# Kernel optimization log

Hardware: AMD Instinct MI355X
Metric: run time of the kernel (lower is better)

Reference implementation:

```python
import jax, jax.numpy as jnp
import numpy as np

N = 20000       # nodes
E = 100000      # edges
STEPS = 4
ND = 128        # node feature dim
ED = 128        # edge feature dim
NIN = 128       # node input dim
EIN = 291       # edge input dim (2 + 17*17)
H = 64          # mpn edge-mlp hidden


def _lin(x, w, b):
    return x @ w + b


def setup_inputs():
    key = jax.random.key(0)
    ks = jax.random.split(key, 16)

    def w(k, i, o):
        return (jax.random.normal(k, (i, o), jnp.float32) / np.float32(np.sqrt(i)))

    d = {}
    d["x"] = jax.random.normal(ks[0], (N, NIN), jnp.float32)
    d["edge_attr"] = jax.random.normal(ks[1], (E, EIN), jnp.float32)
    d["edge_index"] = jax.random.randint(ks[2], (2, E), 0, N, jnp.int32)
    # node embedding MLP: NIN -> 128 -> ND (ReLU between, none after last)
    d["new0"] = w(ks[3], NIN, 128); d["neb0"] = jnp.zeros(128, jnp.float32)
    d["new1"] = w(ks[4], 128, ND); d["neb1"] = jnp.zeros(ND, jnp.float32)
    # edge embedding MLP: EIN -> 64 -> ED
    d["eew0"] = w(ks[5], EIN, 64); d["eeb0"] = jnp.zeros(64, jnp.float32)
    d["eew1"] = w(ks[6], 64, ED); d["eeb1"] = jnp.zeros(ED, jnp.float32)
    # MPN edge MLP (skip=True): 2*(2*ND) + 2*ED = 768 -> 64 -> ED, ReLU after each
    d["mew0"] = w(ks[7], 4 * ND + 2 * ED, H); d["meb0"] = jnp.zeros(H, jnp.float32)
    d["mew1"] = w(ks[8], H, ED); d["meb1"] = jnp.zeros(ED, jnp.float32)
    # MPN node MLP: 2*ND + ED = 384 -> ND, ReLU
    d["mnw0"] = w(ks[9], 2 * ND + ED, ND); d["mnb0"] = jnp.zeros(ND, jnp.float32)
    # classification MLP: ED -> 64 -> 32 -> 1
    d["cw0"] = w(ks[10], ED, 64); d["cb0"] = jnp.zeros(64, jnp.float32)
    d["cw1"] = w(ks[11], 64, 32); d["cb1"] = jnp.zeros(32, jnp.float32)
    d["cw2"] = w(ks[12], 32, 1); d["cb2"] = jnp.zeros(1, jnp.float32)
    return d


def reference(x, edge_attr, edge_index,
              new0, neb0, new1, neb1,
              eew0, eeb0, eew1, eeb1,
              mew0, meb0, mew1, meb1,
              mnw0, mnb0,
              cw0, cb0, cw1, cb1, cw2, cb2):
    relu = jax.nn.relu
    j, i = edge_index[0], edge_index[1]  # j: source, i: target

    nf = _lin(relu(_lin(x, new0, neb0)), new1, neb1)          # [N, ND]
    ef = _lin(relu(_lin(edge_attr, eew0, eeb0)), eew1, eeb1)  # [E, ED]
    nf0, ef0 = nf, ef

    for _ in range(STEPS):
        # skip connections: concat initial features
        nfc = jnp.concatenate([nf0, nf], axis=1)  # [N, 2*ND]
        efc = jnp.concatenate([ef0, ef], axis=1)  # [E, 2*ED]
        x_i = nfc[i]  # [E, 2*ND] target
        x_j = nfc[j]  # [E, 2*ND] source
        # edge update MLP (ReLU after both layers)
        h = relu(_lin(jnp.concatenate([x_i, x_j, efc], axis=1), mew0, meb0))
        ef = relu(_lin(h, mew1, meb1))  # [E, ED]
        # message: mlp_node([x_i, edge_attr_new]) aggregated at target i
        msg = relu(_lin(jnp.concatenate([x_i, ef], axis=1), mnw0, mnb0))  # [E, ND]
        nf = jax.ops.segment_sum(msg, i, num_segments=N)  # [N, ND]

    out = relu(_lin(ef, cw0, cb0))
    out = relu(_lin(out, cw1, cb1))
    out = _lin(out, cw2, cb2)  # [E, 1]
    return out
```

## Files before the change

kernel.cpp:

```cpp
#include <hip/hip_runtime.h>
#include <hip/hip_bf16.h>

#define ND 128
#define ED 128
#define NIN 128
#define EIN 291
#define KPAD 320
#define HH 64
#define TM 32
#define TS 64
#define GSE 768
#define MAXGE 3

typedef __attribute__((ext_vector_type(8))) short short8;
typedef __attribute__((ext_vector_type(4))) float float4_;

__device__ __forceinline__ unsigned short f2bf(float f)
{
    union { float f; unsigned u; } v; v.f = f;
    unsigned u = v.u;
    unsigned r = (u + 0x7FFFu + ((u >> 16) & 1u)) >> 16;
    return (unsigned short)r;
}
__device__ __forceinline__ float bf2f(unsigned short s)
{
    union { unsigned u; float f; } v; v.u = ((unsigned)s) << 16;
    return v.f;
}

template<int T, int KC, int K>
__device__ __forceinline__ void stage_frags(const unsigned short* __restrict__ src,
                                            unsigned short* __restrict__ wreg,
                                            int t, int k0)
{
    constexpr int TOT = T * KC * 64;
#pragma unroll
    for (int it = 0; it < TOT / 256; it++) {
        int idx = it * 256 + t;
        int f = idx >> 6, l = idx & 63;
        int col = (f / KC) * 16 + (l & 15);
        int k = (f % KC) * 32 + ((l >> 4) * 8);
        *(short8*)&wreg[idx * 8] = *(const short8*)&src[(size_t)col * K + k0 + k];
    }
}
#define FRAG(wreg, f, lane) (*(const short8*)&(wreg)[(((f) << 6) + (lane)) * 8])

__global__ __launch_bounds__(256) void zero_k(float* __restrict__ p, int n4)
{
    int idx = blockIdx.x * 256 + threadIdx.x;
    if (idx < n4) ((float4*)p)[idx] = make_float4(0.f, 0.f, 0.f, 0.f);
}

__global__ __launch_bounds__(256) void hist_k(const int* __restrict__ tgti,
                                              int* __restrict__ deg, int E)
{
    int e = blockIdx.x * 256 + threadIdx.x;
    if (e < E) atomicAdd(&deg[tgti[e]], 1);
}

__global__ __launch_bounds__(256) void scan_k(const int* __restrict__ deg,
                                              int* __restrict__ row_ptr,
                                              int* __restrict__ cursor, int N, int E)
{
    __shared__ int part[256];
    const int t = threadIdx.x;
    const int chunk = (N + 255) / 256;
    const int base = t * chunk;
    int s = 0;
    for (int k = 0; k < chunk; k++) { int idx = base + k; if (idx < N) s += deg[idx]; }
    part[t] = s;
    __syncthreads();
    for (int off = 1; off < 256; off <<= 1) {
        int v = (t >= off) ? part[t - off] : 0;
        __syncthreads();
        part[t] += v;
        __syncthreads();
    }
    int run = (t == 0) ? 0 : part[t - 1];
    for (int k = 0; k < chunk; k++) {
        int idx = base + k;
        if (idx < N) { row_ptr[idx] = run; cursor[idx] = run; run += deg[idx]; }
    }
    if (t == 255) row_ptr[N] = E;
}

__global__ __launch_bounds__(256) void scatter_k(const int* __restrict__ tgti,
                                                 int* __restrict__ cursor,
                                                 int* __restrict__ csr_eid, int E)
{
    int e = blockIdx.x * 256 + threadIdx.x;
    if (e < E) {
        int p = atomicAdd(&cursor[tgti[e]], 1);
        csr_eid[p] = e;
    }
}

__global__ __launch_bounds__(256) void permidx_k(const int* __restrict__ csr_eid,
                                                 const int* __restrict__ srcj,
                                                 const int* __restrict__ tgti,
                                                 int* __restrict__ srcp,
                                                 int* __restrict__ tgtp, int E)
{
    int p = blockIdx.x * 256 + threadIdx.x;
    if (p < E) {
        int e = csr_eid[p];
        srcp[p] = srcj[e];
        tgtp[p] = tgti[e];
    }
}

__global__ __launch_bounds__(256) void fixup_k(const int* __restrict__ row_ptr,
                                               float* __restrict__ nfx,
                                               unsigned short* __restrict__ nf_out, int N)
{
    int n = blockIdx.x * 2 + (threadIdx.x >> 7);
    int c = threadIdx.x & 127;
    if (n >= N) return;
    int beg = row_ptr[n], end = row_ptr[n + 1];
    if (beg == end) { nf_out[(size_t)n * ND + c] = 0; return; }
    if ((beg >> 5) != ((end - 1) >> 5)) {
        size_t idx = (size_t)n * ND + c;
        nf_out[idx] = f2bf(nfx[idx]);
        nfx[idx] = 0.f;
    }
}

__global__ __launch_bounds__(256) void wprep_k(
    const float* __restrict__ mew0, const float* __restrict__ mew1, const float* __restrict__ mnw0,
    const float* __restrict__ eew0, const float* __restrict__ eew1, const float* __restrict__ cw0,
    const float* __restrict__ new0, const float* __restrict__ new1,
    unsigned short* __restrict__ w0T, unsigned short* __restrict__ w1T,
    unsigned short* __restrict__ wmT, unsigned short* __restrict__ w0eT,
    unsigned short* __restrict__ w1eT, unsigned short* __restrict__ cw0T,
    unsigned short* __restrict__ w0nT, unsigned short* __restrict__ w1nT)
{
    int idx = blockIdx.x * 256 + threadIdx.x;
    if (idx < 49152) {
        int c = idx / 768, k = idx % 768;
        w0T[idx] = f2bf(mew0[k * 64 + c]);
    } else if (idx < 57344) {
        int j = idx - 49152; int c = j / 64, k = j % 64;
        w1T[j] = f2bf(mew1[k * 128 + c]);
    } else if (idx < 106496) {
        int j = idx - 57344; int c = j / 384, k = j % 384;
        wmT[j] = f2bf(mnw0[k * 128 + c]);
    } else if (idx < 126976) {
        int j = idx - 106496; int c = j / KPAD, k = j % KPAD;
        w0eT[j] = (k < EIN) ? f2bf(eew0[k * 64 + c]) : (unsigned short)0;
    } else if (idx < 135168) {
        int j = idx - 126976; int c = j / 64, k = j % 64;
        w1eT[j] = f2bf(eew1[k * 128 + c]);
    } else if (idx < 143360) {
        int j = idx - 135168; int c = j / 128, k = j % 128;
        cw0T[j] = f2bf(cw0[k * 64 + c]);
    } else if (idx < 159744) {
        int j = idx - 143360; int c = j / 128, k = j % 128;
        w0nT[j] = f2bf(new0[k * 128 + c]);
    } else if (idx < 176128) {
        int j = idx - 159744; int c = j / 128, k = j % 128;
        w1nT[j] = f2bf(new1[k * 128 + c]);
    }
}

__global__ __launch_bounds__(256) void node_embed_k(
    const float* __restrict__ x,
    const unsigned short* __restrict__ w0nT, const float* __restrict__ b0,
    const unsigned short* __restrict__ w1nT, const float* __restrict__ b1,
    unsigned short* __restrict__ nf0_bf, unsigned short* __restrict__ nf_bf, int N)
{
    const int t = threadIdx.x;
    const int n0 = blockIdx.x * TM;
    __shared__ unsigned short wreg[8192];
    __shared__ unsigned short xin[TM][130];
    __shared__ unsigned short h_bf[TM][130];

#pragma unroll
    for (int it = 0; it < 4; it++) {
        int idx = it * 256 + t;
        int r = idx >> 5, c4 = idx & 31;
        int node = n0 + r; if (node >= N) node = N - 1;
        float4 v = *(const float4*)(x + (size_t)node * NIN + c4 * 4);
        unsigned lo = (unsigned)f2bf(v.x) | ((unsigned)f2bf(v.y) << 16);
        unsigned hi = (unsigned)f2bf(v.z) | ((unsigned)f2bf(v.w) << 16);
        *(uint2*)&xin[r][c4 * 4] = make_uint2(lo, hi);
    }

    const int w = t >> 6, lane = t & 63, quad = lane >> 4, n16 = lane & 15;
    const int m = w & 1, nh = w >> 1;

    float4_ acc[4];
#pragma unroll
    for (int q = 0; q < 4; q++) acc[q] = (float4_){0.f, 0.f, 0.f, 0.f};
#pragma unroll
    for (int hf = 0; hf < 2; hf++) {
        stage_frags<8, 2, 128>(w0nT, wreg, t, hf * 64);
        __syncthreads();
#pragma unroll
        for (int kc = 0; kc < 2; kc++) {
            short8 a = *(const short8*)&xin[m * 16 + n16][hf * 64 + kc * 32 + quad * 8];
#pragma unroll
            for (int tt = 0; tt < 4; tt++) {
                short8 b = FRAG(wreg, (nh * 4 + tt) * 2 + kc, lane);
                acc[tt] = __builtin_amdgcn_mfma_f32_16x16x32_bf16(a, b, acc[tt], 0, 0, 0);
            }
        }
        __syncthreads();
    }
#pragma unroll
    for (int tt = 0; tt < 4; tt++) {
        int c = nh * 64 + tt * 16 + n16;
        float bias = b0[c];
#pragma unroll
        for (int r4 = 0; r4 < 4; r4++)
            h_bf[m * 16 + quad * 4 + r4][c] = f2bf(fmaxf(acc[tt][r4] + bias, 0.f));
    }
    __syncthreads();

    float4_ acc2[4];
#pragma unroll
    for (int q = 0; q < 4; q++) acc2[q] = (float4_){0.f, 0.f, 0.f, 0.f};
#pragma unroll
    for (int hf = 0; hf < 2; hf++) {
        stage_frags<8, 2, 128>(w1nT, wreg, t, hf * 64);
        __syncthreads();
#pragma unroll
        for (int kc = 0; kc < 2; kc++) {
            short8 a = *(const short8*)&h_bf[m * 16 + n16][hf * 64 + kc * 32 + quad * 8];
#pragma unroll
            for (int tt = 0; tt < 4; tt++) {
                short8 b = FRAG(wreg, (nh * 4 + tt) * 2 + kc, lane);
                acc2[tt] = __builtin_amdgcn_mfma_f32_16x16x32_bf16(a, b, acc2[tt], 0, 0, 0);
            }
        }
        __syncthreads();
    }
#pragma unroll
    for (int tt = 0; tt < 4; tt++) {
        int c = nh * 64 + tt * 16 + n16;
        float bias = b1[c];
#pragma unroll
        for (int r4 = 0; r4 < 4; r4++) {
            int row = m * 16 + quad * 4 + r4;
            int node = n0 + row;
            if (node < N) {
                unsigned short v = f2bf(acc2[tt][r4] + bias);
                nf0_bf[(size_t)node * ND + c] = v;
                nf_bf[(size_t)node * ND + c] = v;
            }
        }
    }
}

__global__ __launch_bounds__(256, 3) void edge_embed_k(
    const float* __restrict__ ea, const int* __restrict__ csr_eid,
    const unsigned short* __restrict__ w0eT, const float* __restrict__ b0,
    const unsigned short* __restrict__ w1eT, const float* __restrict__ b1,
    unsigned short* __restrict__ ef0_bf, unsigned short* __restrict__ ef_bf,
    int E, int ntiles)
{
    const int t = threadIdx.x;
    __shared__ unsigned short w0reg[10240];
    __shared__ unsigned short w1reg[8192];
    __shared__ unsigned short hsl[4][16 * 66];

    const int w = t >> 6, lane = t & 63, quad = lane >> 4, n16 = lane & 15;

    stage_frags<8, 2, 64>(w1eT, w1reg, t, 0);

    int ng = 0;
    int tile[MAXGE];
#pragma unroll
    for (int g = 0; g < MAXGE; g++) {
        int tl = blockIdx.x + g * GSE;
        if (tl < ntiles) { tile[g] = tl; ng = g + 1; }
        else tile[g] = 0;
    }

    float4_ accL[MAXGE][4];
#pragma unroll
    for (int g = 0; g < MAXGE; g++)
#pragma unroll
        for (int q = 0; q < 4; q++) accL[g][q] = (float4_){0.f, 0.f, 0.f, 0.f};

#pragma unroll
    for (int hf = 0; hf < 2; hf++) {
        __syncthreads();
        stage_frags<4, 5, KPAD>(w0eT, w0reg, t, hf * 160);
        __syncthreads();
#pragma unroll
        for (int g = 0; g < MAXGE; g++) {
            if (g < ng) {
                int p = tile[g] * 64 + w * 16 + n16; if (p >= E) p = E - 1;
                const float* src = ea + (size_t)csr_eid[p] * EIN;
#pragma unroll
                for (int kc = 0; kc < 5; kc++) {
                    int k = hf * 160 + kc * 32 + quad * 8;
                    union { short8 s; uint4 u; } av;
                    if (k + 8 <= EIN) {
                        float4 v0 = *(const float4*)(src + k);
                        float4 v1 = *(const float4*)(src + k + 4);
                        av.u.x = (unsigned)f2bf(v0.x) | ((unsigned)f2bf(v0.y) << 16);
                        av.u.y = (unsigned)f2bf(v0.z) | ((unsigned)f2bf(v0.w) << 16);
                        av.u.z = (unsigned)f2bf(v1.x) | ((unsigned)f2bf(v1.y) << 16);
                        av.u.w = (unsigned)f2bf(v1.z) | ((unsigned)f2bf(v1.w) << 16);
                    } else {
                        unsigned short vv[8];
#pragma unroll
                        for (int j = 0; j < 8; j++)
                            vv[j] = (k + j < EIN) ? f2bf(src[k + j]) : (unsigned short)0;
                        av.u.x = (unsigned)vv[0] | ((unsigned)vv[1] << 16);
                        av.u.y = (unsigned)vv[2] | ((unsigned)vv[3] << 16);
                        av.u.z = (unsigned)vv[4] | ((unsigned)vv[5] << 16);
                        av.u.w = (unsigned)vv[6] | ((unsigned)vv[7] << 16);
                    }
#pragma unroll
                    for (int tt = 0; tt < 4; tt++) {
                        short8 b = FRAG(w0reg, tt * 5 + kc, lane);
                        accL[g][tt] = __builtin_amdgcn_mfma_f32_16x16x32_bf16(av.s, b, accL[g][tt], 0, 0, 0);
                    }
                }
            }
        }
    }

#pragma unroll
    for (int g = 0; g < MAXGE; g++) {
        if (g < ng) {
#pragma unroll
            for (int tt = 0; tt < 4; tt++) {
                int c = tt * 16 + n16;
                float bias = b0[c];
#pragma unroll
                for (int r4 = 0; r4 < 4; r4++)
                    hsl[w][(quad * 4 + r4) * 66 + c] = f2bf(fmaxf(accL[g][tt][r4] + bias, 0.f));
            }
            float4_ acc2[8];
#pragma unroll
            for (int q = 0; q < 8; q++) acc2[q] = (float4_){0.f, 0.f, 0.f, 0.f};
#pragma unroll
            for (int kc = 0; kc < 2; kc++) {
                short8 a2 = *(const short8*)&hsl[w][n16 * 66 + kc * 32 + quad * 8];
#pragma unroll
                for (int tt = 0; tt < 8; tt++)
                    acc2[tt] = __builtin_amdgcn_mfma_f32_16x16x32_bf16(
                        a2, FRAG(w1reg, tt * 2 + kc, lane), acc2[tt], 0, 0, 0);
            }
#pragma unroll
            for (int tt = 0; tt < 8; tt++) {
                int c = tt * 16 + n16;
                float bias = b1[c];
#pragma unroll
                for (int r4 = 0; r4 < 4; r4++) {
                    int p = tile[g] * 64 + w * 16 + quad * 4 + r4;
                    if (p < E) {
                        unsigned short v = f2bf(acc2[tt][r4] + bias);
                        ef0_bf[(size_t)p * ED + c] = v;
                        ef_bf[(size_t)p * ED + c] = v;
                    }
                }
            }
        }
    }
}

__global__ __launch_bounds__(256, 4) void edge_step_k(
    const int* __restrict__ srcp, const int* __restrict__ tgtp,
    const unsigned short* __restrict__ nf0_bf, const unsigned short* __restrict__ nf_in,
    const unsigned short* __restrict__ ef0_bf, unsigned short* __restrict__ ef_bf,
    unsigned short* __restrict__ nf_out, float* __restrict__ nfx,
    const unsigned short* __restrict__ w0T, const float* __restrict__ meb0,
    const unsigned short* __restrict__ w1T, const float* __restrict__ meb1,
    const unsigned short* __restrict__ wmT, const float* __restrict__ mnb0,
    int E, int wmsg)
{
    const int t = threadIdx.x;
    const int e0 = blockIdx.x * TS;
    __shared__ unsigned short wreg[8192];
    __shared__ unsigned short hef[4][2080];

    const int w = t >> 6, lane = t & 63, quad = lane >> 4, n16 = lane & 15;
    int ec = e0 + w * 16 + n16; if (ec >= E) ec = E - 1;
    const int ti = tgtp[ec], sj = srcp[ec];

    const unsigned short* pA[6] = {
        nf0_bf + (size_t)ti * ND + quad * 8,
        nf_in  + (size_t)ti * ND + quad * 8,
        nf0_bf + (size_t)sj * ND + quad * 8,
        nf_in  + (size_t)sj * ND + quad * 8,
        ef0_bf + (size_t)ec * ED + quad * 8,
        ef_bf  + (size_t)ec * ED + quad * 8 };

    float4_ accL[4];
#pragma unroll
    for (int q = 0; q < 4; q++) accL[q] = (float4_){0.f, 0.f, 0.f, 0.f};
#pragma unroll
    for (int hf = 0; hf < 6; hf++) {
        short8 a4[4];
#pragma unroll
        for (int q2 = 0; q2 < 4; q2++)
            a4[q2] = *(const short8*)(pA[hf] + q2 * 32);
        stage_frags<4, 4, 768>(w0T, wreg, t, hf * 128);
        __syncthreads();
#pragma unroll
        for (int kc = 0; kc < 4; kc++) {
#pragma unroll
            for (int tt = 0; tt < 4; tt++) {
                short8 b = FRAG(wreg, tt * 4 + kc, lane);
                accL[tt] = __builtin_amdgcn_mfma_f32_16x16x32_bf16(a4[kc], b, accL[tt], 0, 0, 0);
            }
        }
        __syncthreads();
    }

#pragma unroll
    for (int tt = 0; tt < 4; tt++) {
        int c = tt * 16 + n16;
        float bias = meb0[c];
#pragma unroll
        for (int r4 = 0; r4 < 4; r4++)
            hef[w][(quad * 4 + r4) * 66 + c] = f2bf(fmaxf(accL[tt][r4] + bias, 0.f));
    }

    stage_frags<8, 2, 64>(w1T, wreg, t, 0);
    __syncthreads();
    {
        float4_ acc[8];
#pragma unroll
        for (int q = 0; q < 8; q++) acc[q] = (float4_){0.f, 0.f, 0.f, 0.f};
#pragma unroll
        for (int kc = 0; kc < 2; kc++) {
            short8 a = *(const short8*)&hef[w][n16 * 66 + kc * 32 + quad * 8];
#pragma unroll
            for (int tt = 0; tt < 8; tt++) {
                short8 b = FRAG(wreg, tt * 2 + kc, lane);
                acc[tt] = __builtin_amdgcn_mfma_f32_16x16x32_bf16(a, b, acc[tt], 0, 0, 0);
            }
        }
#pragma unroll
        for (int tt = 0; tt < 8; tt++) {
            int c = tt * 16 + n16;
            float bias = meb1[c];
#pragma unroll
            for (int r4 = 0; r4 < 4; r4++) {
                int row = quad * 4 + r4;
                unsigned short v = f2bf(fmaxf(acc[tt][r4] + bias, 0.f));
                hef[w][row * 130 + c] = v;
                int e = e0 + w * 16 + row;
                if (e < E) ef_bf[(size_t)e * ED + c] = v;
            }
        }
    }
    __syncthreads();

    if (wmsg) {
        float4_ accM[8];
#pragma unroll
        for (int q = 0; q < 8; q++) accM[q] = (float4_){0.f, 0.f, 0.f, 0.f};
#pragma unroll
        for (int j = 0; j < 6; j++) {
            short8 a2[2];
#pragma unroll
            for (int kc = 0; kc < 2; kc++) {
                int kk = j * 2 + kc;
                if (kk < 8) a2[kc] = *(const short8*)(pA[kk >> 2] + (kk & 3) * 32);
                else        a2[kc] = *(const short8*)&hef[w][n16 * 130 + (kk - 8) * 32 + quad * 8];
            }
            stage_frags<8, 2, 384>(wmT, wreg, t, j * 64);
            __syncthreads();
#pragma unroll
            for (int kc = 0; kc < 2; kc++) {
#pragma unroll
                for (int tt = 0; tt < 8; tt++) {
                    short8 b = FRAG(wreg, tt * 2 + kc, lane);
                    accM[tt] = __builtin_amdgcn_mfma_f32_16x16x32_bf16(a2[kc], b, accM[tt], 0, 0, 0);
                }
            }
            __syncthreads();
        }

#pragma unroll
        for (int tt = 0; tt < 8; tt++) {
            int c = tt * 16 + n16;
            float bias = mnb0[c];
#pragma unroll
            for (int r4 = 0; r4 < 4; r4++) {
                int row = w * 16 + quad * 4 + r4;
                wreg[row * 128 + c] = f2bf(fmaxf(accM[tt][r4] + bias, 0.f));
            }
        }
        int* tg = (int*)&hef[0][0];
        if (t < 66) {
            int p = e0 - 1 + t;
            tg[t] = (p >= 0 && p < E) ? tgtp[p] : -1;
        }
        __syncthreads();
        {
            int c = t & 127, half = t >> 7;
            int r0 = half * 32;
            float acc = 0.f;
            int rs = 0;
            for (int r = 0; r < 32; r++) {
                int p = e0 + r0 + r;
                if (p >= E) break;
                int n = tg[r0 + r + 1];
                acc += bf2f(wreg[(r0 + r) * 128 + c]);
                bool end_here = (tg[r0 + r + 2] != n);
                if (end_here) {
                    bool beg_in = (rs > 0) || (tg[r0] != n);
                    if (beg_in) nf_out[(size_t)n * ND + c] = f2bf(acc);
                    else        atomicAdd(&nfx[(size_t)n * ND + c], acc);
                    acc = 0.f; rs = r + 1;
                } else if (r == 31) {
                    atomicAdd(&nfx[(size_t)n * ND + c], acc);
                }
            }
        }
    }
}

__global__ __launch_bounds__(256) void classify_k(
    const unsigned short* __restrict__ ef_bf, const int* __restrict__ csr_eid,
    const unsigned short* __restrict__ cw0T, const float* __restrict__ cb0,
    const float* __restrict__ cw1, const float* __restrict__ cb1,
    const float* __restrict__ cw2, const float* __restrict__ cb2,
    float* __restrict__ out, int E)
{
    const int t = threadIdx.x;
    const int e0 = blockIdx.x * TM;
    __shared__ unsigned short h0_bf[TM][66];
    __shared__ float h1[TM][33];

    const int w = t >> 6, lane = t & 63, quad = lane >> 4, n16 = lane & 15;
    const int m = w & 1;
    const int erow = m * 16 + n16;
    int ec = e0 + erow; if (ec >= E) ec = E - 1;
    const unsigned short* pa = ef_bf + (size_t)ec * ED + quad * 8;

    {
        const int cb = (w >> 1) * 32;
        float4_ acc0 = {0.f, 0.f, 0.f, 0.f}, acc1 = acc0;
        const unsigned short* b0p = cw0T + (size_t)(cb + n16) * 128 + quad * 8;
        const unsigned short* b1p = b0p + (size_t)16 * 128;
#pragma unroll
        for (int kc = 0; kc < 4; kc++) {
            short8 a  = *(const short8*)(pa + kc * 32);
            short8 bb0 = *(const short8*)(b0p + kc * 32);
            short8 bb1 = *(const short8*)(b1p + kc * 32);
            acc0 = __builtin_amdgcn_mfma_f32_16x16x32_bf16(a, bb0, acc0, 0, 0, 0);
            acc1 = __builtin_amdgcn_mfma_f32_16x16x32_bf16(a, bb1, acc1, 0, 0, 0);
        }
#pragma unroll
        for (int t2 = 0; t2 < 2; t2++) {
            int c = cb + t2 * 16 + n16;
            float bias = cb0[c];
            float4_ ac = t2 ? acc1 : acc0;
#pragma unroll
            for (int r4 = 0; r4 < 4; r4++)
                h0_bf[m * 16 + quad * 4 + r4][c] = f2bf(fmaxf(ac[r4] + bias, 0.f));
        }
    }
    __syncthreads();

    {
        int c = t & 31;
        int rbase = (t >> 5) * 4;
#pragma unroll
        for (int q = 0; q < 4; q++) {
            int r = rbase + q;
            float acc = cb1[c];
#pragma unroll 8
            for (int k = 0; k < 64; k++) acc += bf2f(h0_bf[r][k]) * cw1[k * 32 + c];
            h1[r][c] = fmaxf(acc, 0.f);
        }
    }
    __syncthreads();

    if (t < TM) {
        int p = e0 + t;
        if (p < E) {
            float a = cb2[0];
#pragma unroll
            for (int k = 0; k < 32; k++) a += h1[t][k] * cw2[k];
            out[csr_eid[p]] = a;
        }
    }
}

extern "C" void kernel_launch(void* const* d_in, const int* in_sizes, int n_in,
                              void* d_out, int out_size, void* d_ws, size_t ws_size,
                              hipStream_t stream)
{
    const float* x    = (const float*)d_in[0];
    const float* ea   = (const float*)d_in[1];
    const int*   eidx = (const int*)d_in[2];
    const float* new0 = (const float*)d_in[3];  const float* neb0 = (const float*)d_in[4];
    const float* new1 = (const float*)d_in[5];  const float* neb1 = (const float*)d_in[6];
    const float* eew0 = (const float*)d_in[7];  const float* eeb0 = (const float*)d_in[8];
    const float* eew1 = (const float*)d_in[9];  const float* eeb1 = (const float*)d_in[10];
    const float* mew0 = (const float*)d_in[11]; const float* meb0 = (const float*)d_in[12];
    const float* mew1 = (const float*)d_in[13]; const float* meb1 = (const float*)d_in[14];
    const float* mnw0 = (const float*)d_in[15]; const float* mnb0 = (const float*)d_in[16];
    const float* cw0  = (const float*)d_in[17]; const float* cb0  = (const float*)d_in[18];
    const float* cw1  = (const float*)d_in[19]; const float* cb1  = (const float*)d_in[20];
    const float* cw2  = (const float*)d_in[21]; const float* cb2  = (const float*)d_in[22];

    const int N = in_sizes[0] / NIN;
    const int E = in_sizes[2] / 2;
    const int* srcj = eidx;
    const int* tgti = eidx + E;

    char* wsb = (char*)d_ws;
    unsigned short* nf0_bf = (unsigned short*)wsb;
    unsigned short* nfA    = nf0_bf + (size_t)N * ND;
    unsigned short* ef0_bf = nfA + (size_t)N * ND;
    unsigned short* ef_bf  = ef0_bf + (size_t)E * ED;
    unsigned short* slot   = ef_bf + (size_t)E * ED;
    unsigned short* nfB    = slot;
    float*          nfx    = (float*)(slot + (size_t)N * ND);
    unsigned short* w0T  = slot + (size_t)E * ND;
    unsigned short* w1T  = w0T + 49152;
    unsigned short* wmT  = w1T + 8192;
    unsigned short* w0eT = wmT + 49152;
    unsigned short* w1eT = w0eT + 64 * KPAD;
    unsigned short* cw0T = w1eT + 8192;
    unsigned short* w0nT = cw0T + 8192;
    unsigned short* w1nT = w0nT + 16384;
    int* deg     = (int*)(w1nT + 16384);
    int* cursor  = deg + N;
    int* row_ptr = cursor + N;
    int* csr_eid = row_ptr + (N + 4);
    int* srcp    = csr_eid + E;
    int* tgtp    = srcp + E;

    const int eblocks32 = (E + TM - 1) / TM;
    const int nblocks32 = (N + TM - 1) / TM;
    const int ntiles64 = (E + 63) / 64;

    wprep_k<<<(176128 + 255) / 256, 256, 0, stream>>>(mew0, mew1, mnw0, eew0, eew1, cw0,
                                                      new0, new1,
                                                      w0T, w1T, wmT, w0eT, w1eT, cw0T,
                                                      w0nT, w1nT);

    zero_k<<<((2 * N) / 4 + 255) / 256, 256, 0, stream>>>((float*)deg, (2 * N) / 4);
    hist_k<<<(E + 255) / 256, 256, 0, stream>>>(tgti, deg, E);
    scan_k<<<1, 256, 0, stream>>>(deg, row_ptr, cursor, N, E);
    scatter_k<<<(E + 255) / 256, 256, 0, stream>>>(tgti, cursor, csr_eid, E);
    permidx_k<<<(E + 255) / 256, 256, 0, stream>>>(csr_eid, srcj, tgti, srcp, tgtp, E);

    zero_k<<<((N * ND) / 4 + 255) / 256, 256, 0, stream>>>(nfx, (N * ND) / 4);

    node_embed_k<<<nblocks32, 256, 0, stream>>>(x, w0nT, neb0, w1nT, neb1,
                                                nf0_bf, nfA, N);
    edge_embed_k<<<GSE, 256, 0, stream>>>(ea, csr_eid, w0eT, eeb0, w1eT, eeb1,
                                          ef0_bf, ef_bf, E, ntiles64);

    unsigned short* nfR = nfA;
    unsigned short* nfW = nfB;
    for (int s = 0; s < 4; s++) {
        edge_step_k<<<ntiles64, 256, 0, stream>>>(srcp, tgtp, nf0_bf, nfR,
                                                  ef0_bf, ef_bf, nfW, nfx,
                                                  w0T, meb0, w1T, meb1, wmT, mnb0,
                                                  E, (s < 3) ? 1 : 0);
        if (s < 3) {
            fixup_k<<<(N + 1) / 2, 256, 0, stream>>>(row_ptr, nfx, nfW, N);
            unsigned short* tmp = nfR; nfR = nfW; nfW = tmp;
        }
    }

    classify_k<<<eblocks32, 256, 0, stream>>>(ef_bf, csr_eid, cw0T, cb0, cw1, cb1, cw2, cb2,
                                              (float*)d_out, E);
}
```

Before: 664.0 us.

## Merge node and edge embedding kernels and fold setup launches together

Several launches are combined. The deg zeroing moves into the weight-prep kernel, the permuted-index writes move into the scatter kernel, and node and edge embedding become one kernel that picks its branch by block index and shares one shared-memory buffer. The goal is to cut launch count and gaps between kernels, and to let the small node-embedding work run beside the edge embedding. One catch is that the fused embed kernel carries the edge path's launch bound of 3 and its larger shared-memory footprint, which may lower occupancy for the node blocks.

```diff
diff --git a/kernel.cpp b/kernel.cpp
--- a/kernel.cpp
+++ b/kernel.cpp
@@ -84,28 +84,20 @@
     if (t == 255) row_ptr[N] = E;
 }
 
-__global__ __launch_bounds__(256) void scatter_k(const int* __restrict__ tgti,
+__global__ __launch_bounds__(256) void scatter_k(const int* __restrict__ srcj,
+                                                 const int* __restrict__ tgti,
                                                  int* __restrict__ cursor,
-                                                 int* __restrict__ csr_eid, int E)
+                                                 int* __restrict__ csr_eid,
+                                                 int* __restrict__ srcp,
+                                                 int* __restrict__ tgtp, int E)
 {
     int e = blockIdx.x * 256 + threadIdx.x;
     if (e < E) {
-        int p = atomicAdd(&cursor[tgti[e]], 1);
+        int tg = tgti[e];
+        int p = atomicAdd(&cursor[tg], 1);
         csr_eid[p] = e;
-    }
-}
-
-__global__ __launch_bounds__(256) void permidx_k(const int* __restrict__ csr_eid,
-                                                 const int* __restrict__ srcj,
-                                                 const int* __restrict__ tgti,
-                                                 int* __restrict__ srcp,
-                                                 int* __restrict__ tgtp, int E)
-{
-    int p = blockIdx.x * 256 + threadIdx.x;
-    if (p < E) {
-        int e = csr_eid[p];
         srcp[p] = srcj[e];
-        tgtp[p] = tgti[e];
+        tgtp[p] = tg;
     }
 }
 
@@ -132,7 +124,8 @@
     unsigned short* __restrict__ w0T, unsigned short* __restrict__ w1T,
     unsigned short* __restrict__ wmT, unsigned short* __restrict__ w0eT,
     unsigned short* __restrict__ w1eT, unsigned short* __restrict__ cw0T,
-    unsigned short* __restrict__ w0nT, unsigned short* __restrict__ w1nT)
+    unsigned short* __restrict__ w0nT, unsigned short* __restrict__ w1nT,
+    int* __restrict__ deg, int N)
 {
     int idx = blockIdx.x * 256 + threadIdx.x;
     if (idx < 49152) {
@@ -159,204 +152,204 @@
     } else if (idx < 176128) {
         int j = idx - 159744; int c = j / 128, k = j % 128;
         w1nT[j] = f2bf(new1[k * 128 + c]);
-    }
-}
-
-__global__ __launch_bounds__(256) void node_embed_k(
+    } else if (idx < 176128 + N) {
+        deg[idx - 176128] = 0;
+    }
+}
+
+__global__ __launch_bounds__(256, 3) void embed_k(
+    const float* __restrict__ ea, const int* __restrict__ csr_eid,
+    const unsigned short* __restrict__ w0eT, const float* __restrict__ eb0,
+    const unsigned short* __restrict__ w1eT, const float* __restrict__ eb1,
+    unsigned short* __restrict__ ef0_bf, unsigned short* __restrict__ ef_bf,
+    int E, int ntiles,
     const float* __restrict__ x,
-    const unsigned short* __restrict__ w0nT, const float* __restrict__ b0,
-    const unsigned short* __restrict__ w1nT, const float* __restrict__ b1,
+    const unsigned short* __restrict__ w0nT, const float* __restrict__ nb0,
+    const unsigned short* __restrict__ w1nT, const float* __restrict__ nb1,
     unsigned short* __restrict__ nf0_bf, unsigned short* __restrict__ nf_bf, int N)
 {
+    __shared__ unsigned short smem[22656];
     const int t = threadIdx.x;
-    const int n0 = blockIdx.x * TM;
-    __shared__ unsigned short wreg[8192];
-    __shared__ unsigned short xin[TM][130];
-    __shared__ unsigned short h_bf[TM][130];
-
-#pragma unroll
-    for (int it = 0; it < 4; it++) {
-        int idx = it * 256 + t;
-        int r = idx >> 5, c4 = idx & 31;
-        int node = n0 + r; if (node >= N) node = N - 1;
-        float4 v = *(const float4*)(x + (size_t)node * NIN + c4 * 4);
-        unsigned lo = (unsigned)f2bf(v.x) | ((unsigned)f2bf(v.y) << 16);
-        unsigned hi = (unsigned)f2bf(v.z) | ((unsigned)f2bf(v.w) << 16);
-        *(uint2*)&xin[r][c4 * 4] = make_uint2(lo, hi);
-    }
-
     const int w = t >> 6, lane = t & 63, quad = lane >> 4, n16 = lane & 15;
-    const int m = w & 1, nh = w >> 1;
-
-    float4_ acc[4];
-#pragma unroll
-    for (int q = 0; q < 4; q++) acc[q] = (float4_){0.f, 0.f, 0.f, 0.f};
-#pragma unroll
-    for (int hf = 0; hf < 2; hf++) {
-        stage_frags<8, 2, 128>(w0nT, wreg, t, hf * 64);
-        __syncthreads();
-#pragma unroll
-        for (int kc = 0; kc < 2; kc++) {
-            short8 a = *(const short8*)&xin[m * 16 + n16][hf * 64 + kc * 32 + quad * 8];
-#pragma unroll
-            for (int tt = 0; tt < 4; tt++) {
-                short8 b = FRAG(wreg, (nh * 4 + tt) * 2 + kc, lane);
-                acc[tt] = __builtin_amdgcn_mfma_f32_16x16x32_bf16(a, b, acc[tt], 0, 0, 0);
-            }
-        }
-        __syncthreads();
-    }
-#pragma unroll
-    for (int tt = 0; tt < 4; tt++) {
-        int c = nh * 64 + tt * 16 + n16;
-        float bias = b0[c];
-#pragma unroll
-        for (int r4 = 0; r4 < 4; r4++)
-            h_bf[m * 16 + quad * 4 + r4][c] = f2bf(fmaxf(acc[tt][r4] + bias, 0.f));
-    }
-    __syncthreads();
-
-    float4_ acc2[4];
-#pragma unroll
-    for (int q = 0; q < 4; q++) acc2[q] = (float4_){0.f, 0.f, 0.f, 0.f};
-#pragma unroll
-    for (int hf = 0; hf < 2; hf++) {
-        stage_frags<8, 2, 128>(w1nT, wreg, t, hf * 64);
-        __syncthreads();
-#pragma unroll
-        for (int kc = 0; kc < 2; kc++) {
-            short8 a = *(const short8*)&h_bf[m * 16 + n16][hf * 64 + kc * 32 + quad * 8];
-#pragma unroll
-            for (int tt = 0; tt < 4; tt++) {
-                short8 b = FRAG(wreg, (nh * 4 + tt) * 2 + kc, lane);
-                acc2[tt] = __builtin_amdgcn_mfma_f32_16x16x32_bf16(a, b, acc2[tt], 0, 0, 0);
-            }
-        }
-        __syncthreads();
-    }
-#pragma unroll
-    for (int tt = 0; tt < 4; tt++) {
-        int c = nh * 64 + tt * 16 + n16;
-        float bias = b1[c];
-#pragma unroll
-        for (int r4 = 0; r4 < 4; r4++) {
-            int row = m * 16 + quad * 4 + r4;
-            int node = n0 + row;
-            if (node < N) {
-                unsigned short v = f2bf(acc2[tt][r4] + bias);
-                nf0_bf[(size_t)node * ND + c] = v;
-                nf_bf[(size_t)node * ND + c] = v;
-            }
-        }
-    }
-}
-
-__global__ __launch_bounds__(256, 3) void edge_embed_k(
-    const float* __restrict__ ea, const int* __restrict__ csr_eid,
-    const unsigned short* __restrict__ w0eT, const float* __restrict__ b0,
-    const unsigned short* __restrict__ w1eT, const float* __restrict__ b1,
-    unsigned short* __restrict__ ef0_bf, unsigned short* __restrict__ ef_bf,
-    int E, int ntiles)
-{
-    const int t = threadIdx.x;
-    __shared__ unsigned short w0reg[10240];
-    __shared__ unsigned short w1reg[8192];
-    __shared__ unsigned short hsl[4][16 * 66];
-
-    const int w = t >> 6, lane = t & 63, quad = lane >> 4, n16 = lane & 15;
-
-    stage_frags<8, 2, 64>(w1eT, w1reg, t, 0);
-
-    int ng = 0;
-    int tile[MAXGE];
-#pragma unroll
-    for (int g = 0; g < MAXGE; g++) {
-        int tl = blockIdx.x + g * GSE;
-        if (tl < ntiles) { tile[g] = tl; ng = g + 1; }
-        else tile[g] = 0;
-    }
-
-    float4_ accL[MAXGE][4];
-#pragma unroll
-    for (int g = 0; g < MAXGE; g++)
-#pragma unroll
-        for (int q = 0; q < 4; q++) accL[g][q] = (float4_){0.f, 0.f, 0.f, 0.f};
-
-#pragma unroll
-    for (int hf = 0; hf < 2; hf++) {
-        __syncthreads();
-        stage_frags<4, 5, KPAD>(w0eT, w0reg, t, hf * 160);
-        __syncthreads();
+
+    if (blockIdx.x < GSE) {
+        unsigned short* w0reg = smem;
+        unsigned short* w1reg = smem + 10240;
+        unsigned short* hsl   = smem + 18432;
+
+        stage_frags<8, 2, 64>(w1eT, w1reg, t, 0);
+
+        int ng = 0;
+        int tile[MAXGE];
+#pragma unroll
+        for (int g = 0; g < MAXGE; g++) {
+            int tl = blockIdx.x + g * GSE;
+            if (tl < ntiles) { tile[g] = tl; ng = g + 1; }
+            else tile[g] = 0;
+        }
+
+        float4_ accL[MAXGE][4];
+#pragma unroll
+        for (int g = 0; g < MAXGE; g++)
+#pragma unroll
+            for (int q = 0; q < 4; q++) accL[g][q] = (float4_){0.f, 0.f, 0.f, 0.f};
+
+#pragma unroll
+        for (int hf = 0; hf < 2; hf++) {
+            __syncthreads();
+            stage_frags<4, 5, KPAD>(w0eT, w0reg, t, hf * 160);
+            __syncthreads();
+#pragma unroll
+            for (int g = 0; g < MAXGE; g++) {
+                if (g < ng) {
+                    int p = tile[g] * 64 + w * 16 + n16; if (p >= E) p = E - 1;
+                    const float* src = ea + (size_t)csr_eid[p] * EIN;
+#pragma unroll
+                    for (int kc = 0; kc < 5; kc++) {
+                        int k = hf * 160 + kc * 32 + quad * 8;
+                        union { short8 s; uint4 u; } av;
+                        if (k + 8 <= EIN) {
+                            float4 v0 = *(const float4*)(src + k);
+                            float4 v1 = *(const float4*)(src + k + 4);
+                            av.u.x = (unsigned)f2bf(v0.x) | ((unsigned)f2bf(v0.y) << 16);
+                            av.u.y = (unsigned)f2bf(v0.z) | ((unsigned)f2bf(v0.w) << 16);
+                            av.u.z = (unsigned)f2bf(v1.x) | ((unsigned)f2bf(v1.y) << 16);
+                            av.u.w = (unsigned)f2bf(v1.z) | ((unsigned)f2bf(v1.w) << 16);
+                        } else {
+                            unsigned short vv[8];
+#pragma unroll
+                            for (int j = 0; j < 8; j++)
+                                vv[j] = (k + j < EIN) ? f2bf(src[k + j]) : (unsigned short)0;
+                            av.u.x = (unsigned)vv[0] | ((unsigned)vv[1] << 16);
+                            av.u.y = (unsigned)vv[2] | ((unsigned)vv[3] << 16);
+                            av.u.z = (unsigned)vv[4] | ((unsigned)vv[5] << 16);
+                            av.u.w = (unsigned)vv[6] | ((unsigned)vv[7] << 16);
+                        }
+#pragma unroll
+                        for (int tt = 0; tt < 4; tt++) {
+                            short8 b = FRAG(w0reg, tt * 5 + kc, lane);
+                            accL[g][tt] = __builtin_amdgcn_mfma_f32_16x16x32_bf16(av.s, b, accL[g][tt], 0, 0, 0);
+                        }
+                    }
+                }
+            }
+        }
+
 #pragma unroll
         for (int g = 0; g < MAXGE; g++) {
             if (g < ng) {
-                int p = tile[g] * 64 + w * 16 + n16; if (p >= E) p = E - 1;
-                const float* src = ea + (size_t)csr_eid[p] * EIN;
-#pragma unroll
-                for (int kc = 0; kc < 5; kc++) {
-                    int k = hf * 160 + kc * 32 + quad * 8;
-                    union { short8 s; uint4 u; } av;
-                    if (k + 8 <= EIN) {
-                        float4 v0 = *(const float4*)(src + k);
-                        float4 v1 = *(const float4*)(src + k + 4);
-                        av.u.x = (unsigned)f2bf(v0.x) | ((unsigned)f2bf(v0.y) << 16);
-                        av.u.y = (unsigned)f2bf(v0.z) | ((unsigned)f2bf(v0.w) << 16);
-                        av.u.z = (unsigned)f2bf(v1.x) | ((unsigned)f2bf(v1.y) << 16);
-                        av.u.w = (unsigned)f2bf(v1.z) | ((unsigned)f2bf(v1.w) << 16);
-                    } else {
-                        unsigned short vv[8];
-#pragma unroll
-                        for (int j = 0; j < 8; j++)
-                            vv[j] = (k + j < EIN) ? f2bf(src[k + j]) : (unsigned short)0;
-                        av.u.x = (unsigned)vv[0] | ((unsigned)vv[1] << 16);
-                        av.u.y = (unsigned)vv[2] | ((unsigned)vv[3] << 16);
-                        av.u.z = (unsigned)vv[4] | ((unsigned)vv[5] << 16);
-                        av.u.w = (unsigned)vv[6] | ((unsigned)vv[7] << 16);
+#pragma unroll
+                for (int tt = 0; tt < 4; tt++) {
+                    int c = tt * 16 + n16;
+                    float bias = eb0[c];
+#pragma unroll
+                    for (int r4 = 0; r4 < 4; r4++)
+                        hsl[w * 1056 + (quad * 4 + r4) * 66 + c] = f2bf(fmaxf(accL[g][tt][r4] + bias, 0.f));
+                }
+                float4_ acc2[8];
+#pragma unroll
+                for (int q = 0; q < 8; q++) acc2[q] = (float4_){0.f, 0.f, 0.f, 0.f};
+#pragma unroll
+                for (int kc = 0; kc < 2; kc++) {
+                    short8 a2 = *(const short8*)&hsl[w * 1056 + n16 * 66 + kc * 32 + quad * 8];
+#pragma unroll
+                    for (int tt = 0; tt < 8; tt++)
+                        acc2[tt] = __builtin_amdgcn_mfma_f32_16x16x32_bf16(
+                            a2, FRAG(w1reg, tt * 2 + kc, lane), acc2[tt], 0, 0, 0);
+                }
+#pragma unroll
+                for (int tt = 0; tt < 8; tt++) {
+                    int c = tt * 16 + n16;
+                    float bias = eb1[c];
+#pragma unroll
+                    for (int r4 = 0; r4 < 4; r4++) {
+                        int p = tile[g] * 64 + w * 16 + quad * 4 + r4;
+                        if (p < E) {
+                            unsigned short v = f2bf(acc2[tt][r4] + bias);
+                            ef0_bf[(size_t)p * ED + c] = v;
+                            ef_bf[(size_t)p * ED + c] = v;
+                        }
                     }
-#pragma unroll
-                    for (int tt = 0; tt < 4; tt++) {
-                        short8 b = FRAG(w0reg, tt * 5 + kc, lane);
-                        accL[g][tt] = __builtin_amdgcn_mfma_f32_16x16x32_bf16(av.s, b, accL[g][tt], 0, 0, 0);
-                    }
-                }
-            }
-        }
-    }
-
-#pragma unroll
-    for (int g = 0; g < MAXGE; g++) {
-        if (g < ng) {
-#pragma unroll
-            for (int tt = 0; tt < 4; tt++) {
-                int c = tt * 16 + n16;
-                float bias = b0[c];
-#pragma unroll
-                for (int r4 = 0; r4 < 4; r4++)
-                    hsl[w][(quad * 4 + r4) * 66 + c] = f2bf(fmaxf(accL[g][tt][r4] + bias, 0.f));
-            }
-            float4_ acc2[8];
-#pragma unroll
-            for (int q = 0; q < 8; q++) acc2[q] = (float4_){0.f, 0.f, 0.f, 0.f};
+                }
+            }
+        }
+    } else {
+        unsigned short* wreg = smem;
+        unsigned short* xin  = smem + 8192;
+        unsigned short* h_bf = smem + 12352;
+        const int n0 = (blockIdx.x - GSE) * TM;
+
+#pragma unroll
+        for (int it = 0; it < 4; it++) {
+            int idx = it * 256 + t;
+            int r = idx >> 5, c4 = idx & 31;
+            int node = n0 + r; if (node >= N) node = N - 1;
+            float4 v = *(const float4*)(x + (size_t)node * NIN + c4 * 4);
+            unsigned lo = (unsigned)f2bf(v.x) | ((unsigned)f2bf(v.y) << 16);
+            unsigned hi = (unsigned)f2bf(v.z) | ((unsigned)f2bf(v.w) << 16);
+            *(uint2*)&xin[r * 130 + c4 * 4] = make_uint2(lo, hi);
+        }
+
+        const int m = w & 1, nh = w >> 1;
+
+        float4_ acc[4];
+#pragma unroll
+        for (int q = 0; q < 4; q++) acc[q] = (float4_){0.f, 0.f, 0.f, 0.f};
+#pragma unroll
+        for (int hf = 0; hf < 2; hf++) {
+            stage_frags<8, 2, 128>(w0nT, wreg, t, hf * 64);
+            __syncthreads();
 #pragma unroll
             for (int kc = 0; kc < 2; kc++) {
-                short8 a2 = *(const short8*)&hsl[w][n16 * 66 + kc * 32 + quad * 8];
-#pragma unroll
-                for (int tt = 0; tt < 8; tt++)
-                    acc2[tt] = __builtin_amdgcn_mfma_f32_16x16x32_bf16(
-                        a2, FRAG(w1reg, tt * 2 + kc, lane), acc2[tt], 0, 0, 0);
-            }
-#pragma unroll
-            for (int tt = 0; tt < 8; tt++) {
-                int c = tt * 16 + n16;
-                float bias = b1[c];
-#pragma unroll
-                for (int r4 = 0; r4 < 4; r4++) {
-                    int p = tile[g] * 64 + w * 16 + quad * 4 + r4;
-                    if (p < E) {
-                        unsigned short v = f2bf(acc2[tt][r4] + bias);
-                        ef0_bf[(size_t)p * ED + c] = v;
-                        ef_bf[(size_t)p * ED + c] = v;
-                    }
+                short8 a = *(const short8*)&xin[(m * 16 + n16) * 130 + hf * 64 + kc * 32 + quad * 8];
+#pragma unroll
+                for (int tt = 0; tt < 4; tt++) {
+                    short8 b = FRAG(wreg, (nh * 4 + tt) * 2 + kc, lane);
+                    acc[tt] = __builtin_amdgcn_mfma_f32_16x16x32_bf16(a, b, acc[tt], 0, 0, 0);
+                }
+            }
+            __syncthreads();
+        }
+#pragma unroll
+        for (int tt = 0; tt < 4; tt++) {
+            int c = nh * 64 + tt * 16 + n16;
+            float bias = nb0[c];
+#pragma unroll
+            for (int r4 = 0; r4 < 4; r4++)
+                h_bf[(m * 16 + quad * 4 + r4) * 130 + c] = f2bf(fmaxf(acc[tt][r4] + bias, 0.f));
+        }
+        __syncthreads();
+
+        float4_ acc2[4];
+#pragma unroll
+        for (int q = 0; q < 4; q++) acc2[q] = (float4_){0.f, 0.f, 0.f, 0.f};
+#pragma unroll
+        for (int hf = 0; hf < 2; hf++) {
+            stage_frags<8, 2, 128>(w1nT, wreg, t, hf * 64);
+            __syncthreads();
+#pragma unroll
+            for (int kc = 0; kc < 2; kc++) {
+                short8 a = *(const short8*)&h_bf[(m * 16 + n16) * 130 + hf * 64 + kc * 32 + quad * 8];
+#pragma unroll
+                for (int tt = 0; tt < 4; tt++) {
+                    short8 b = FRAG(wreg, (nh * 4 + tt) * 2 + kc, lane);
+                    acc2[tt] = __builtin_amdgcn_mfma_f32_16x16x32_bf16(a, b, acc2[tt], 0, 0, 0);
+                }
+            }
+            __syncthreads();
+        }
+#pragma unroll
+        for (int tt = 0; tt < 4; tt++) {
+            int c = nh * 64 + tt * 16 + n16;
+            float bias = nb1[c];
+#pragma unroll
+            for (int r4 = 0; r4 < 4; r4++) {
+                int row = m * 16 + quad * 4 + r4;
+                int node = n0 + row;
+                if (node < N) {
+                    unsigned short v = f2bf(acc2[tt][r4] + bias);
+                    nf0_bf[(size_t)node * ND + c] = v;
+                    nf_bf[(size_t)node * ND + c] = v;
                 }
             }
         }
@@ -636,23 +629,21 @@
     const int nblocks32 = (N + TM - 1) / TM;
     const int ntiles64 = (E + 63) / 64;
 
-    wprep_k<<<(176128 + 255) / 256, 256, 0, stream>>>(mew0, mew1, mnw0, eew0, eew1, cw0,
-                                                      new0, new1,
-                                                      w0T, w1T, wmT, w0eT, w1eT, cw0T,
-                                                      w0nT, w1nT);
-
-    zero_k<<<((2 * N) / 4 + 255) / 256, 256, 0, stream>>>((float*)deg, (2 * N) / 4);
+    wprep_k<<<(176128 + N + 255) / 256, 256, 0, stream>>>(mew0, mew1, mnw0, eew0, eew1, cw0,
+                                                          new0, new1,
+                                                          w0T, w1T, wmT, w0eT, w1eT, cw0T,
+                                                          w0nT, w1nT, deg, N);
+
     hist_k<<<(E + 255) / 256, 256, 0, stream>>>(tgti, deg, E);
     scan_k<<<1, 256, 0, stream>>>(deg, row_ptr, cursor, N, E);
-    scatter_k<<<(E + 255) / 256, 256, 0, stream>>>(tgti, cursor, csr_eid, E);
-    permidx_k<<<(E + 255) / 256, 256, 0, stream>>>(csr_eid, srcj, tgti, srcp, tgtp, E);
+    scatter_k<<<(E + 255) / 256, 256, 0, stream>>>(srcj, tgti, cursor, csr_eid, srcp, tgtp, E);
 
     zero_k<<<((N * ND) / 4 + 255) / 256, 256, 0, stream>>>(nfx, (N * ND) / 4);
 
-    node_embed_k<<<nblocks32, 256, 0, stream>>>(x, w0nT, neb0, w1nT, neb1,
-                                                nf0_bf, nfA, N);
-    edge_embed_k<<<GSE, 256, 0, stream>>>(ea, csr_eid, w0eT, eeb0, w1eT, eeb1,
-                                          ef0_bf, ef_bf, E, ntiles64);
+    embed_k<<<GSE + nblocks32, 256, 0, stream>>>(ea, csr_eid, w0eT, eeb0, w1eT, eeb1,
+                                                 ef0_bf, ef_bf, E, ntiles64,
+                                                 x, w0nT, neb0, w1nT, neb1,
+                                                 nf0_bf, nfA, N);
 
     unsigned short* nfR = nfA;
     unsigned short* nfW = nfB;
```

Result: faster. 645.2 us (-2.8%).
